# Kernel tuning notes

Hardware: AMD Instinct MI355X
Metric: run time of the kernel (lower is better)

Reference implementation:

```python
import jax, jax.numpy as jnp
import numpy as np

# Convex_f forward. D and mid are fixed tridiagonal matrices:
#   (D x)[i]   = -x[i-1] + 2*x[i] - x[i+1]  for 1 <= i <= n-2, and 0 at i=0, n-1
#   (mid x)[i] = 0.5*(x[i-1] + x[i+1])      for 1 <= i <= n-2,
#                0.5*x[1] at i=0, 0.5*x[n-2] at i=n-1
# We implement these as direct 3-point stencils (same math as the dense matmuls).

B, N, K = 256, 8192, 16

def setup_inputs() -> dict:
    key = jax.random.key(0)
    k1, k2 = jax.random.split(key)
    x = jax.random.normal(k1, (B, N, K), dtype=jnp.float32)
    param = jax.random.normal(k2, (B, N, K), dtype=jnp.float32)
    return {"x": x, "param": param}

def _convex_step(y):
    # y: [B, N, K]
    up, ctr, dn = y[:, :-2], y[:, 1:-1], y[:, 2:]
    Dy_in = -up + 2.0 * ctr - dn                      # interior rows of D @ y
    Dy = jnp.pad(Dy_in, ((0, 0), (1, 1), (0, 0)))     # rows 0 and N-1 zeroed
    mid_y = jnp.concatenate(
        [0.5 * y[:, 1:2], 0.5 * (up + dn), 0.5 * y[:, -2:-1]], axis=1
    )                                                 # mid @ y
    dy = (Dy > 0).astype(y.dtype) * (y - mid_y)
    return y - dy

def reference(x, param):
    y = x + param
    return _convex_step(y) - param
```

## Files before the change

kernel.cpp:

```cpp
#include <hip/hip_runtime.h>


#define B_    256
#define N_    8192
#define K_    16
#define TILE  64
#define KQ    4
#define NTILES (N_ / TILE)

__global__ __launch_bounds__(256)
void convex_kernel(const float4* __restrict__ x4,
                   const float4* __restrict__ p4,
                   float4* __restrict__ o4)
{
    __shared__ float4 ysh[TILE + 2][KQ];

    const int tid = threadIdx.x;
    const int row = tid >> 2;
    const int col = tid & 3;
    const int blk = blockIdx.x;
    const int t   = blk & (NTILES - 1);
    const int b   = blk >> 7;
    const int n0  = t * TILE;

    const long base = ((long)b * N_ + n0) * KQ;
    const long idx  = base + (long)row * KQ + col;

    float4 xv = x4[idx];
    float4 pv = p4[idx];
    float4 yv = make_float4(xv.x + pv.x, xv.y + pv.y, xv.z + pv.z, xv.w + pv.w);
    ysh[row + 1][col] = yv;

    if (tid < 8) {
        const int c = tid & 3;
        float4 h = make_float4(0.f, 0.f, 0.f, 0.f);
        if (tid < 4) {
            if (n0 > 0) {
                float4 hx = x4[base - KQ + c];
                float4 hp = p4[base - KQ + c];
                h = make_float4(hx.x + hp.x, hx.y + hp.y, hx.z + hp.z, hx.w + hp.w);
            }
            ysh[0][c] = h;
        } else {
            if (n0 + TILE < N_) {
                float4 hx = x4[base + (long)TILE * KQ + c];
                float4 hp = p4[base + (long)TILE * KQ + c];
                h = make_float4(hx.x + hp.x, hx.y + hp.y, hx.z + hp.z, hx.w + hp.w);
            }
            ysh[TILE + 1][c] = h;
        }
    }
    __syncthreads();

    const int n = n0 + row;
    float4 r;
    if (n == 0 || n == N_ - 1) {
        r = make_float4(yv.x - pv.x, yv.y - pv.y, yv.z - pv.z, yv.w - pv.w);
    } else {
        float4 a = ysh[row][col];
        float4 d = ysh[row + 2][col];
        float4 m = make_float4(0.5f * (a.x + d.x), 0.5f * (a.y + d.y),
                               0.5f * (a.z + d.z), 0.5f * (a.w + d.w));
        r = make_float4(fminf(yv.x, m.x) - pv.x,
                        fminf(yv.y, m.y) - pv.y,
                        fminf(yv.z, m.z) - pv.z,
                        fminf(yv.w, m.w) - pv.w);
    }
    o4[idx] = r;
}

extern "C" void kernel_launch(void* const* d_in, const int* in_sizes, int n_in,
                              void* d_out, int out_size, void* d_ws, size_t ws_size,
                              hipStream_t stream)
{
    const float4* x = (const float4*)d_in[0];
    const float4* p = (const float4*)d_in[1];
    float4*       o = (float4*)d_out;

    dim3 grid(B_ * NTILES);
    dim3 block(256);
    convex_kernel<<<grid, block, 0, stream>>>(x, p, o);
}
```

Before: 299.7 us.

## Process eight rows per thread in registers, drop shared-memory halo

Each thread now handles a strip of eight consecutive rows for one float4 column and holds the stencil window in registers. The shared-memory tile and __syncthreads are removed, and each thread loads its own top and bottom halo rows. This cuts block count and synchronisation, but each thread-strip re-reads two halo rows, adding about 25% extra global reads. Per-thread accesses are strided by 64 bytes across rows, which may hurt coalescing per instruction.

New measurement: 308.9 us. 1.03x slower.

```diff
diff --git a/kernel.cpp b/kernel.cpp
--- a/kernel.cpp
+++ b/kernel.cpp
@@ -1,72 +1,76 @@
 #include <hip/hip_runtime.h>
 
 
-#define B_    256
-#define N_    8192
-#define K_    16
-#define TILE  64
-#define KQ    4
-#define NTILES (N_ / TILE)
+#define B_   256
+#define N_   8192
+#define KQ   4
+#define R_   8
+#define TPB  256
+#define ROWS_PER_BLK ((TPB / KQ) * R_)
+#define TILES (N_ / ROWS_PER_BLK)
 
-__global__ __launch_bounds__(256)
+static_assert(TILES == 16, "b = blk >> 4 assumes 16 tiles");
+
+__device__ __forceinline__ float4 f4add(float4 a, float4 b) {
+    return make_float4(a.x + b.x, a.y + b.y, a.z + b.z, a.w + b.w);
+}
+
+__global__ __launch_bounds__(TPB)
 void convex_kernel(const float4* __restrict__ x4,
                    const float4* __restrict__ p4,
                    float4* __restrict__ o4)
 {
-    __shared__ float4 ysh[TILE + 2][KQ];
+    const int tid = threadIdx.x;
+    const int c   = tid & (KQ - 1);
+    const int g   = tid >> 2;
+    const int blk = blockIdx.x;
+    const int t   = blk & (TILES - 1);
+    const int b   = blk >> 4;
+    const int n0  = t * ROWS_PER_BLK + g * R_;
 
-    const int tid = threadIdx.x;
-    const int row = tid >> 2;
-    const int col = tid & 3;
-    const int blk = blockIdx.x;
-    const int t   = blk & (NTILES - 1);
-    const int b   = blk >> 7;
-    const int n0  = t * TILE;
+    const int base = (b * N_ + n0) * KQ + c;
 
-    const long base = ((long)b * N_ + n0) * KQ;
-    const long idx  = base + (long)row * KQ + col;
+    const int topI = (n0 > 0)        ? base - KQ       : base;
+    const int botI = (n0 + R_ < N_)  ? base + R_ * KQ  : base;
 
-    float4 xv = x4[idx];
-    float4 pv = p4[idx];
-    float4 yv = make_float4(xv.x + pv.x, xv.y + pv.y, xv.z + pv.z, xv.w + pv.w);
-    ysh[row + 1][col] = yv;
+    float4 xt = x4[topI];
+    float4 pt = p4[topI];
+    float4 xb = x4[botI];
+    float4 pb = p4[botI];
 
-    if (tid < 8) {
-        const int c = tid & 3;
-        float4 h = make_float4(0.f, 0.f, 0.f, 0.f);
-        if (tid < 4) {
-            if (n0 > 0) {
-                float4 hx = x4[base - KQ + c];
-                float4 hp = p4[base - KQ + c];
-                h = make_float4(hx.x + hp.x, hx.y + hp.y, hx.z + hp.z, hx.w + hp.w);
-            }
-            ysh[0][c] = h;
+    float4 xv[R_], pv[R_];
+#pragma unroll
+    for (int j = 0; j < R_; ++j) {
+        xv[j] = x4[base + j * KQ];
+        pv[j] = p4[base + j * KQ];
+    }
+
+    float4 y[R_ + 2];
+    y[0] = f4add(xt, pt);
+#pragma unroll
+    for (int j = 0; j < R_; ++j) y[j + 1] = f4add(xv[j], pv[j]);
+    y[R_ + 1] = f4add(xb, pb);
+
+#pragma unroll
+    for (int j = 0; j < R_; ++j) {
+        const int n = n0 + j;
+        const float4 yc = y[j + 1];
+        const float4 p  = pv[j];
+        float4 r;
+        if (n == 0 || n == N_ - 1) {
+            r = make_float4(yc.x - p.x, yc.y - p.y, yc.z - p.z, yc.w - p.w);
         } else {
-            if (n0 + TILE < N_) {
-                float4 hx = x4[base + (long)TILE * KQ + c];
-                float4 hp = p4[base + (long)TILE * KQ + c];
-                h = make_float4(hx.x + hp.x, hx.y + hp.y, hx.z + hp.z, hx.w + hp.w);
-            }
-            ysh[TILE + 1][c] = h;
+            const float4 a = y[j];
+            const float4 d = y[j + 2];
+            const float4 m = make_float4(0.5f * (a.x + d.x), 0.5f * (a.y + d.y),
+                                         0.5f * (a.z + d.z), 0.5f * (a.w + d.w));
+            r = make_float4(fminf(yc.x, m.x) - p.x,
+                            fminf(yc.y, m.y) - p.y,
+                            fminf(yc.z, m.z) - p.z,
+                            fminf(yc.w, m.w) - p.w);
         }
+        o4[base + j * KQ] = r;
     }
-    __syncthreads();
-
-    const int n = n0 + row;
-    float4 r;
-    if (n == 0 || n == N_ - 1) {
-        r = make_float4(yv.x - pv.x, yv.y - pv.y, yv.z - pv.z, yv.w - pv.w);
-    } else {
-        float4 a = ysh[row][col];
-        float4 d = ysh[row + 2][col];
-        float4 m = make_float4(0.5f * (a.x + d.x), 0.5f * (a.y + d.y),
-                               0.5f * (a.z + d.z), 0.5f * (a.w + d.w));
-        r = make_float4(fminf(yv.x, m.x) - pv.x,
-                        fminf(yv.y, m.y) - pv.y,
-                        fminf(yv.z, m.z) - pv.z,
-                        fminf(yv.w, m.w) - pv.w);
-    }
-    o4[idx] = r;
 }
 
 extern "C" void kernel_launch(void* const* d_in, const int* in_sizes, int n_in,
@@ -77,7 +81,7 @@
     const float4* p = (const float4*)d_in[1];
     float4*       o = (float4*)d_out;
 
-    dim3 grid(B_ * NTILES);
-    dim3 block(256);
+    dim3 grid(B_ * TILES);
+    dim3 block(TPB);
     convex_kernel<<<grid, block, 0, stream>>>(x, p, o);
 }
```

## Replace LDS-tiled stencil with persistent per-wave streaming and neighbor reloads

Applied to the files above, without the earlier changes.

Drops the shared-memory tile and the __syncthreads. Each wave now walks a contiguous span of rows in a grid-stride loop and loads the up and down neighbors straight from global memory, relying on cache hits. The grid shrinks to 2048 blocks so fewer, longer-lived workgroups stream the data. The cost is three times the load instructions per output, which must be served by L1/L2 to avoid extra DRAM traffic.

Measured after the change: 321.5 us. 1.07x slower.

```diff
diff --git a/kernel.cpp b/kernel.cpp
--- a/kernel.cpp
+++ b/kernel.cpp
@@ -3,70 +3,69 @@
 
 #define B_    256
 #define N_    8192
-#define K_    16
-#define TILE  64
 #define KQ    4
-#define NTILES (N_ / TILE)
+#define TPB   256
+#define GRID  2048
+#define WPB   (TPB / 64)
+#define NWAVES (GRID * WPB)
+#define WAVES_PER_B (NWAVES / B_)
+#define SPAN  (N_ / WAVES_PER_B)
+#define NSTEP (SPAN / 16)
 
-__global__ __launch_bounds__(256)
+static_assert(NWAVES % B_ == 0, "wave/batch split");
+static_assert(N_ % WAVES_PER_B == 0, "span split");
+
+__global__ __launch_bounds__(TPB)
 void convex_kernel(const float4* __restrict__ x4,
                    const float4* __restrict__ p4,
                    float4* __restrict__ o4)
 {
-    __shared__ float4 ysh[TILE + 2][KQ];
+    const int tid = threadIdx.x;
+    const int w   = tid >> 6;
+    const int l   = tid & 63;
+    const int g   = l >> 2;
+    const int wid = blockIdx.x * WPB + w;
+    const int b   = wid >> 5;
+    const int s   = (wid & 31) * SPAN;
 
-    const int tid = threadIdx.x;
-    const int row = tid >> 2;
-    const int col = tid & 3;
-    const int blk = blockIdx.x;
-    const int t   = blk & (NTILES - 1);
-    const int b   = blk >> 7;
-    const int n0  = t * TILE;
+    int idx = (b * N_ + s) * KQ + l;
 
-    const long base = ((long)b * N_ + n0) * KQ;
-    const long idx  = base + (long)row * KQ + col;
+#pragma unroll 2
+    for (int i = 0; i < NSTEP; ++i, idx += 16 * KQ) {
+        const int n  = s + i * 16 + g;
+        const bool e0 = (n == 0);
+        const bool e1 = (n == N_ - 1);
+        const int ia = e0 ? idx : idx - KQ;
+        const int id = e1 ? idx : idx + KQ;
 
-    float4 xv = x4[idx];
-    float4 pv = p4[idx];
-    float4 yv = make_float4(xv.x + pv.x, xv.y + pv.y, xv.z + pv.z, xv.w + pv.w);
-    ysh[row + 1][col] = yv;
+        const float4 xc = x4[idx];
+        const float4 pc = p4[idx];
+        const float4 xa = x4[ia];
+        const float4 pa = p4[ia];
+        const float4 xd = x4[id];
+        const float4 pd = p4[id];
 
-    if (tid < 8) {
-        const int c = tid & 3;
-        float4 h = make_float4(0.f, 0.f, 0.f, 0.f);
-        if (tid < 4) {
-            if (n0 > 0) {
-                float4 hx = x4[base - KQ + c];
-                float4 hp = p4[base - KQ + c];
-                h = make_float4(hx.x + hp.x, hx.y + hp.y, hx.z + hp.z, hx.w + hp.w);
-            }
-            ysh[0][c] = h;
-        } else {
-            if (n0 + TILE < N_) {
-                float4 hx = x4[base + (long)TILE * KQ + c];
-                float4 hp = p4[base + (long)TILE * KQ + c];
-                h = make_float4(hx.x + hp.x, hx.y + hp.y, hx.z + hp.z, hx.w + hp.w);
-            }
-            ysh[TILE + 1][c] = h;
+        const float4 yc = make_float4(xc.x + pc.x, xc.y + pc.y,
+                                      xc.z + pc.z, xc.w + pc.w);
+        const float4 ya = make_float4(xa.x + pa.x, xa.y + pa.y,
+                                      xa.z + pa.z, xa.w + pa.w);
+        const float4 yd = make_float4(xd.x + pd.x, xd.y + pd.y,
+                                      xd.z + pd.z, xd.w + pd.w);
+
+        const bool edge = e0 | e1;
+        float4 r;
+        {
+            const float mx = 0.5f * (ya.x + yd.x);
+            const float my = 0.5f * (ya.y + yd.y);
+            const float mz = 0.5f * (ya.z + yd.z);
+            const float mw = 0.5f * (ya.w + yd.w);
+            r.x = (edge ? yc.x : fminf(yc.x, mx)) - pc.x;
+            r.y = (edge ? yc.y : fminf(yc.y, my)) - pc.y;
+            r.z = (edge ? yc.z : fminf(yc.z, mz)) - pc.z;
+            r.w = (edge ? yc.w : fminf(yc.w, mw)) - pc.w;
         }
+        o4[idx] = r;
     }
-    __syncthreads();
-
-    const int n = n0 + row;
-    float4 r;
-    if (n == 0 || n == N_ - 1) {
-        r = make_float4(yv.x - pv.x, yv.y - pv.y, yv.z - pv.z, yv.w - pv.w);
-    } else {
-        float4 a = ysh[row][col];
-        float4 d = ysh[row + 2][col];
-        float4 m = make_float4(0.5f * (a.x + d.x), 0.5f * (a.y + d.y),
-                               0.5f * (a.z + d.z), 0.5f * (a.w + d.w));
-        r = make_float4(fminf(yv.x, m.x) - pv.x,
-                        fminf(yv.y, m.y) - pv.y,
-                        fminf(yv.z, m.z) - pv.z,
-                        fminf(yv.w, m.w) - pv.w);
-    }
-    o4[idx] = r;
 }
 
 extern "C" void kernel_launch(void* const* d_in, const int* in_sizes, int n_in,
@@ -77,7 +76,7 @@
     const float4* p = (const float4*)d_in[1];
     float4*       o = (float4*)d_out;
 
-    dim3 grid(B_ * NTILES);
-    dim3 block(256);
+    dim3 grid(GRID);
+    dim3 block(TPB);
     convex_kernel<<<grid, block, 0, stream>>>(x, p, o);
 }
```
